# Performance work log

Hardware: AMD Instinct MI355X
Metric: run time of the kernel (lower is better)

The kernel has to match this reference:

```python
import jax, jax.numpy as jnp
import numpy as np

N_HEAD = 16

def setup_inputs() -> dict:
    key = jax.random.key(0)
    ks = jax.random.split(key, 5)
    B, S, D = 2, 2048, 1024
    x = jax.random.normal(ks[0], (B, S, D), dtype=jnp.float32)
    w_attn = jax.random.normal(ks[1], (3 * D, D), dtype=jnp.float32) * 0.02
    b_attn = jax.random.normal(ks[2], (3 * D,), dtype=jnp.float32) * 0.02
    w_proj = jax.random.normal(ks[3], (D, D), dtype=jnp.float32) * 0.02
    b_proj = jax.random.normal(ks[4], (D,), dtype=jnp.float32) * 0.02
    return {"x": x, "w_attn": w_attn, "b_attn": b_attn, "w_proj": w_proj, "b_proj": b_proj}

def reference(x, w_attn, b_attn, w_proj, b_proj):
    B, S, D = x.shape
    H = N_HEAD
    hd = D // H
    # QKV projection (nn.Linear: x @ W^T + b)
    qkv = x @ w_attn.T + b_attn  # [B, S, 3D]
    q, k, v = jnp.split(qkv, 3, axis=2)
    q = q.reshape(B, S, H, hd).transpose(0, 2, 1, 3)  # [B, H, S, hd]
    k = k.reshape(B, S, H, hd).transpose(0, 2, 1, 3)
    v = v.reshape(B, S, H, hd).transpose(0, 2, 1, 3)
    scale = 1.0 / jnp.sqrt(jnp.asarray(hd, dtype=x.dtype))
    attn = jnp.einsum("bhqd,bhkd->bhqk", q, k) * scale  # [B, H, S, S]
    causal = jnp.tril(jnp.ones((S, S), dtype=bool))
    attn = jnp.where(causal[None, None], attn, -jnp.inf)
    attn = jax.nn.softmax(attn, axis=-1)
    y = jnp.einsum("bhqk,bhkd->bhqd", attn, v)  # [B, H, S, hd]
    y = y.transpose(0, 2, 1, 3).reshape(B, S, D)
    return y @ w_proj.T + b_proj
```

## Files before the change

### kernel.cpp

```cpp
#include <hip/hip_runtime.h>
#include <hip/hip_bf16.h>

#define S_LEN 2048
#define DMODEL 1024
#define NHEAD 16
#define HD 64

typedef short short8 __attribute__((ext_vector_type(8)));
typedef short short4_t __attribute__((ext_vector_type(4)));
typedef float f32x4 __attribute__((ext_vector_type(4)));

__device__ inline unsigned short f2bf(float f) {
    union { float f; unsigned int u; } c;
    c.f = f;
    unsigned int r = c.u + 0x7fffu + ((c.u >> 16) & 1u);
    return (unsigned short)(r >> 16);
}

__global__ __launch_bounds__(256) void cast_f32_bf16(
    const float* __restrict__ in, short* __restrict__ out, int n8)
{
    int i = blockIdx.x * 256 + threadIdx.x;
    if (i < n8) {
        float4 a = ((const float4*)in)[2 * i];
        float4 b = ((const float4*)in)[2 * i + 1];
        short8 o;
        o[0] = (short)f2bf(a.x); o[1] = (short)f2bf(a.y);
        o[2] = (short)f2bf(a.z); o[3] = (short)f2bf(a.w);
        o[4] = (short)f2bf(b.x); o[5] = (short)f2bf(b.y);
        o[6] = (short)f2bf(b.z); o[7] = (short)f2bf(b.w);
        ((short8*)out)[i] = o;
    }
}

template<bool QKV>
__global__ __launch_bounds__(256) void gemm_mfma(
    const short* __restrict__ A, const short* __restrict__ W,
    const float* __restrict__ bias, float* __restrict__ C,
    int N, int K,
    short* __restrict__ qo, short* __restrict__ ko, short* __restrict__ vo)
{
    __shared__ __align__(16) short Ash[128 * 64];
    __shared__ __align__(16) short Bsh[128 * 64];

    const int tid = threadIdx.x;
    const int l = tid & 63;
    const int wid = tid >> 6;
    const int wr = wid >> 1, wc = wid & 1;
    const int n0 = blockIdx.x << 7, m0 = blockIdx.y << 7;

    const short* Abase = A + (size_t)m0 * K;
    const short* Wbase = W + (size_t)n0 * K;

    f32x4 acc[4][4];
    #pragma unroll
    for (int i = 0; i < 4; ++i)
        #pragma unroll
        for (int j = 0; j < 4; ++j)
            acc[i][j] = (f32x4)0.0f;

    short8 sa[4], sb[4];
    int rrow[4], rcol[4];
    #pragma unroll
    for (int i = 0; i < 4; ++i) {
        int chunk = i * 256 + tid;
        rrow[i] = chunk >> 3;
        rcol[i] = (chunk & 7) << 3;
    }

    #pragma unroll
    for (int i = 0; i < 4; ++i) {
        sa[i] = *(const short8*)(Abase + (size_t)rrow[i] * K + rcol[i]);
        sb[i] = *(const short8*)(Wbase + (size_t)rrow[i] * K + rcol[i]);
    }

    const int NT = K >> 6;
    for (int kt = 0; kt < NT; ++kt) {
        __syncthreads();
        #pragma unroll
        for (int i = 0; i < 4; ++i) {
            *(short8*)&Ash[rrow[i] * 64 + rcol[i]] = sa[i];
            *(short8*)&Bsh[rrow[i] * 64 + rcol[i]] = sb[i];
        }
        __syncthreads();
        if (kt + 1 < NT) {
            const int k0 = (kt + 1) << 6;
            #pragma unroll
            for (int i = 0; i < 4; ++i) {
                sa[i] = *(const short8*)(Abase + (size_t)rrow[i] * K + k0 + rcol[i]);
                sb[i] = *(const short8*)(Wbase + (size_t)rrow[i] * K + k0 + rcol[i]);
            }
        }
        #pragma unroll
        for (int kk = 0; kk < 2; ++kk) {
            short8 af[4], bf[4];
            const int kof = kk * 32 + ((l >> 4) << 3);
            #pragma unroll
            for (int mi = 0; mi < 4; ++mi)
                af[mi] = *(const short8*)&Ash[(wr * 64 + mi * 16 + (l & 15)) * 64 + kof];
            #pragma unroll
            for (int ni = 0; ni < 4; ++ni)
                bf[ni] = *(const short8*)&Bsh[(wc * 64 + ni * 16 + (l & 15)) * 64 + kof];
            #pragma unroll
            for (int mi = 0; mi < 4; ++mi)
                #pragma unroll
                for (int ni = 0; ni < 4; ++ni)
                    acc[mi][ni] = __builtin_amdgcn_mfma_f32_16x16x32_bf16(
                        af[mi], bf[ni], acc[mi][ni], 0, 0, 0);
        }
    }

    #pragma unroll
    for (int ni = 0; ni < 4; ++ni) {
        const int col = n0 + wc * 64 + ni * 16 + (l & 15);
        const float bv = bias[col];
        if (QKV) {
            const int part = col >> 10;
            const int h = (col >> 6) & 15;
            const int e = col & 63;
            short* __restrict__ dst = part == 0 ? qo : (part == 1 ? ko : vo);
            #pragma unroll
            for (int mi = 0; mi < 4; ++mi) {
                #pragma unroll
                for (int r = 0; r < 4; ++r) {
                    int row = m0 + wr * 64 + mi * 16 + ((l >> 4) << 2) + r;
                    int b = row >> 11, s = row & (S_LEN - 1);
                    dst[((size_t)(b * NHEAD + h) * S_LEN + s) * HD + e] =
                        (short)f2bf(acc[mi][ni][r] + bv);
                }
            }
        } else {
            #pragma unroll
            for (int mi = 0; mi < 4; ++mi) {
                #pragma unroll
                for (int r = 0; r < 4; ++r) {
                    int row = m0 + wr * 64 + mi * 16 + ((l >> 4) << 2) + r;
                    C[(size_t)row * N + col] = acc[mi][ni][r] + bv;
                }
            }
        }
    }
}

__global__ __launch_bounds__(256) void transpose_v(
    const short* __restrict__ vin, short* __restrict__ vout)
{
    __shared__ short t[64][72];
    const int tid = threadIdx.x;
    const int bh = blockIdx.x >> 5;
    const int s0 = (blockIdx.x & 31) << 6;
    const size_t ibase = (size_t)bh * S_LEN * HD;
    const size_t obase = (size_t)bh * HD * S_LEN;
    const int r = tid >> 3, c8 = (tid & 7) << 3;

    #pragma unroll
    for (int p = 0; p < 2; ++p) {
        short8 v = *(const short8*)&vin[ibase + (size_t)(s0 + r + p * 32) * HD + c8];
        *(short8*)&t[r + p * 32][c8] = v;
    }
    __syncthreads();
    #pragma unroll
    for (int p = 0; p < 2; ++p) {
        const int e = r + p * 32;
        short8 o;
        #pragma unroll
        for (int i = 0; i < 8; ++i) o[i] = t[c8 + i][e];
        *(short8*)&vout[obase + (size_t)e * S_LEN + s0 + c8] = o;
    }
}

__global__ __launch_bounds__(256) void flash_attn_mfma(
    const short* __restrict__ q, const short* __restrict__ k,
    const short* __restrict__ vt, short* __restrict__ yb)
{
    __shared__ __align__(16) short Ks[64 * 64];
    __shared__ __align__(16) short Vs[64 * 64];

    const int tid = threadIdx.x;
    const int l = tid & 63;
    const int w = tid >> 6;
    const int h4 = l >> 4;
    const int c15 = l & 15;
    const int bid = blockIdx.x;
    const int qt = 31 - (bid >> 5);
    const int bh = bid & 31;
    const int q0 = qt << 6;
    const int myq = q0 + (w << 4) + c15;

    const size_t kbase = (size_t)bh * S_LEN * HD;
    const size_t vbase = (size_t)bh * HD * S_LEN;

    short8 qf[2];
    {
        const short* qrow = q + kbase + (size_t)myq * HD;
        qf[0] = *(const short8*)(qrow + (h4 << 3));
        qf[1] = *(const short8*)(qrow + 32 + (h4 << 3));
    }

    f32x4 accO[4];
    #pragma unroll
    for (int i = 0; i < 4; ++i) accO[i] = (f32x4)0.0f;
    float mr = -1e30f, lr = 0.0f;

    const int srow0 = tid >> 3, scol = tid & 7;
    short8 kreg[2], vreg[2];
    #pragma unroll
    for (int p = 0; p < 2; ++p) {
        kreg[p] = *(const short8*)(k + kbase + (size_t)(srow0 + p * 32) * HD + scol * 8);
        vreg[p] = *(const short8*)(vt + vbase + (size_t)(srow0 + p * 32) * S_LEN + scol * 8);
    }

    const int ntiles = qt + 1;
    for (int t = 0; t < ntiles; ++t) {
        __syncthreads();
        #pragma unroll
        for (int p = 0; p < 2; ++p) {
            const int row = srow0 + p * 32;
            const int sc = (scol ^ (row & 7)) << 3;
            *(short8*)&Ks[row * 64 + sc] = kreg[p];
            *(short8*)&Vs[row * 64 + sc] = vreg[p];
        }
        __syncthreads();
        if (t + 1 < ntiles) {
            const int kn = (t + 1) << 6;
            #pragma unroll
            for (int p = 0; p < 2; ++p) {
                kreg[p] = *(const short8*)(k + kbase + (size_t)(kn + srow0 + p * 32) * HD + scol * 8);
                vreg[p] = *(const short8*)(vt + vbase + (size_t)(srow0 + p * 32) * S_LEN + kn + scol * 8);
            }
        }

        f32x4 sacc[4];
        #pragma unroll
        for (int nt = 0; nt < 4; ++nt) sacc[nt] = (f32x4)0.0f;
        #pragma unroll
        for (int c = 0; c < 2; ++c) {
            const int kof = (c << 5) + (h4 << 3);
            #pragma unroll
            for (int nt = 0; nt < 4; ++nt) {
                const int keyrow = nt * 16 + c15;
                const short8 kf = *(const short8*)&Ks[keyrow * 64 + (kof ^ ((keyrow & 7) << 3))];
                sacc[nt] = __builtin_amdgcn_mfma_f32_16x16x32_bf16(kf, qf[c], sacc[nt], 0, 0, 0);
            }
        }

        float p16[16];
        const bool diag = (t == qt);
        #pragma unroll
        for (int nt = 0; nt < 4; ++nt)
            #pragma unroll
            for (int r = 0; r < 4; ++r) {
                float v = sacc[nt][r] * 0.125f;
                if (diag && (nt * 16 + (h4 << 2) + r > (w << 4) + c15))
                    v = -1e30f;
                p16[nt * 4 + r] = v;
            }

        float mx = p16[0];
        #pragma unroll
        for (int i = 1; i < 16; ++i) mx = fmaxf(mx, p16[i]);
        mx = fmaxf(mx, __shfl_xor(mx, 16, 64));
        mx = fmaxf(mx, __shfl_xor(mx, 32, 64));
        const float mnew = fmaxf(mr, mx);
        const float alpha = __expf(mr - mnew);
        mr = mnew;
        float rs = 0.0f;
        #pragma unroll
        for (int i = 0; i < 16; ++i) {
            p16[i] = __expf(p16[i] - mnew);
            rs += p16[i];
        }
        rs += __shfl_xor(rs, 16, 64);
        rs += __shfl_xor(rs, 32, 64);
        lr = lr * alpha + rs;
        #pragma unroll
        for (int et = 0; et < 4; ++et) accO[et] *= alpha;

        short8 pb[2];
        #pragma unroll
        for (int c = 0; c < 2; ++c)
            #pragma unroll
            for (int i = 0; i < 8; ++i)
                pb[c][i] = (short)f2bf(p16[8 * c + i]);

        #pragma unroll
        for (int c = 0; c < 2; ++c) {
            const int ch = (c << 2) + (h4 >> 1);
            const int halfo = (h4 & 1) << 2;
            #pragma unroll
            for (int et = 0; et < 4; ++et) {
                const int e = (et << 4) + c15;
                const int rb = e << 6;
                const int sw = e & 7;
                const short4_t va = *(const short4_t*)&Vs[rb + ((ch ^ sw) << 3) + halfo];
                const short4_t vb = *(const short4_t*)&Vs[rb + (((ch + 2) ^ sw) << 3) + halfo];
                const short8 vf = {va[0], va[1], va[2], va[3], vb[0], vb[1], vb[2], vb[3]};
                accO[et] = __builtin_amdgcn_mfma_f32_16x16x32_bf16(vf, pb[c], accO[et], 0, 0, 0);
            }
        }
    }

    const int bq = bh >> 4, hh = bh & 15;
    const float inv = 1.0f / lr;
    short* orow = yb + ((size_t)bq * S_LEN + myq) * DMODEL + hh * HD;
    #pragma unroll
    for (int et = 0; et < 4; ++et) {
        short4_t o;
        #pragma unroll
        for (int r = 0; r < 4; ++r) o[r] = (short)f2bf(accO[et][r] * inv);
        *(short4_t*)&orow[(et << 4) + (h4 << 2)] = o;
    }
}

extern "C" void kernel_launch(void* const* d_in, const int* in_sizes, int n_in,
                              void* d_out, int out_size, void* d_ws, size_t ws_size,
                              hipStream_t stream) {
    const float* x      = (const float*)d_in[0];
    const float* w_attn = (const float*)d_in[1];
    const float* b_attn = (const float*)d_in[2];
    const float* w_proj = (const float*)d_in[3];
    const float* b_proj = (const float*)d_in[4];
    float* out = (float*)d_out;

    const int B = 2;
    const int M = B * S_LEN;
    const size_t x_elems  = (size_t)M * DMODEL;
    const size_t wa_elems = (size_t)3 * DMODEL * DMODEL;
    const size_t wp_elems = (size_t)DMODEL * DMODEL;

    char* wsb = (char*)d_ws;
    short* qw  = (short*)(wsb);
    short* kw  = (short*)(wsb + (8u << 20));
    short* vw  = (short*)(wsb + (16u << 20));
    short* vtw = (short*)(wsb + (24u << 20));
    short* xb  = (short*)(wsb + (32u << 20));
    short* yb  = (short*)(wsb + (32u << 20));
    short* wab = (short*)(wsb + (40u << 20));
    short* wpb = (short*)(wsb + (40u << 20));

    cast_f32_bf16<<<dim3((int)(x_elems  / 8 / 256)), 256, 0, stream>>>(x, xb, (int)(x_elems / 8));
    cast_f32_bf16<<<dim3((int)(wa_elems / 8 / 256)), 256, 0, stream>>>(w_attn, wab, (int)(wa_elems / 8));

    dim3 g1(3 * DMODEL / 128, M / 128);
    gemm_mfma<true><<<g1, 256, 0, stream>>>(xb, wab, b_attn, nullptr,
                                            3 * DMODEL, DMODEL, qw, kw, vw);

    cast_f32_bf16<<<dim3((int)(wp_elems / 8 / 256)), 256, 0, stream>>>(w_proj, wpb, (int)(wp_elems / 8));
    transpose_v<<<dim3(2 * NHEAD * (S_LEN / 64)), 256, 0, stream>>>(vw, vtw);

    flash_attn_mfma<<<dim3(2 * NHEAD * (S_LEN / 64)), 256, 0, stream>>>(qw, kw, vtw, yb);

    dim3 g3(DMODEL / 128, M / 128);
    gemm_mfma<false><<<g3, 256, 0, stream>>>(yb, wpb, b_proj, out,
                                             DMODEL, DMODEL,
                                             nullptr, nullptr, nullptr);
}
```

Before: 200.7 us.

## Load GEMM and attention tiles directly into LDS and skip unneeded softmax rescales

Replaces register-staged global-to-LDS copies in both the GEMM and attention kernels with direct global_load_lds transfers, using an XOR swizzle applied on the global address side so the LDS layout stays conflict-free. This drops the register prefetch of the next tile, so loads are no longer overlapped with compute across iterations; each tile load is now waited on before compute. The GEMM LDS reads are updated to match the new swizzle. The online softmax skips the alpha rescale of the accumulator and running sum when no lane's max increased, using a wave-wide vote.

```diff
diff --git a/kernel.cpp b/kernel.cpp
--- a/kernel.cpp
+++ b/kernel.cpp
@@ -9,6 +9,11 @@
 typedef short short8 __attribute__((ext_vector_type(8)));
 typedef short short4_t __attribute__((ext_vector_type(4)));
 typedef float f32x4 __attribute__((ext_vector_type(4)));
+
+#define GLOAD_LDS16(gp, lp)                                        \
+    __builtin_amdgcn_global_load_lds(                              \
+        (__attribute__((address_space(1))) void*)(gp),             \
+        (__attribute__((address_space(3))) void*)(lp), 16, 0, 0)
 
 __device__ inline unsigned short f2bf(float f) {
     union { float f; unsigned int u; } c;
@@ -59,48 +64,40 @@
         for (int j = 0; j < 4; ++j)
             acc[i][j] = (f32x4)0.0f;
 
-    short8 sa[4], sb[4];
-    int rrow[4], rcol[4];
+    int rrow[4], scol[4];
     #pragma unroll
     for (int i = 0; i < 4; ++i) {
         int chunk = i * 256 + tid;
         rrow[i] = chunk >> 3;
-        rcol[i] = (chunk & 7) << 3;
-    }
-
-    #pragma unroll
-    for (int i = 0; i < 4; ++i) {
-        sa[i] = *(const short8*)(Abase + (size_t)rrow[i] * K + rcol[i]);
-        sb[i] = *(const short8*)(Wbase + (size_t)rrow[i] * K + rcol[i]);
+        scol[i] = ((chunk & 7) ^ (rrow[i] & 7)) << 3;
     }
 
     const int NT = K >> 6;
     for (int kt = 0; kt < NT; ++kt) {
+        const int k0 = kt << 6;
         __syncthreads();
         #pragma unroll
         for (int i = 0; i < 4; ++i) {
-            *(short8*)&Ash[rrow[i] * 64 + rcol[i]] = sa[i];
-            *(short8*)&Bsh[rrow[i] * 64 + rcol[i]] = sb[i];
+            GLOAD_LDS16(Abase + (size_t)rrow[i] * K + k0 + scol[i],
+                        &Ash[(i * 256 + wid * 64) * 8]);
+            GLOAD_LDS16(Wbase + (size_t)rrow[i] * K + k0 + scol[i],
+                        &Bsh[(i * 256 + wid * 64) * 8]);
         }
         __syncthreads();
-        if (kt + 1 < NT) {
-            const int k0 = (kt + 1) << 6;
-            #pragma unroll
-            for (int i = 0; i < 4; ++i) {
-                sa[i] = *(const short8*)(Abase + (size_t)rrow[i] * K + k0 + rcol[i]);
-                sb[i] = *(const short8*)(Wbase + (size_t)rrow[i] * K + k0 + rcol[i]);
-            }
-        }
         #pragma unroll
         for (int kk = 0; kk < 2; ++kk) {
             short8 af[4], bf[4];
-            const int kof = kk * 32 + ((l >> 4) << 3);
-            #pragma unroll
-            for (int mi = 0; mi < 4; ++mi)
-                af[mi] = *(const short8*)&Ash[(wr * 64 + mi * 16 + (l & 15)) * 64 + kof];
-            #pragma unroll
-            for (int ni = 0; ni < 4; ++ni)
-                bf[ni] = *(const short8*)&Bsh[(wc * 64 + ni * 16 + (l & 15)) * 64 + kof];
+            const int slotg = (kk << 2) + (l >> 4);
+            #pragma unroll
+            for (int mi = 0; mi < 4; ++mi) {
+                const int row = wr * 64 + mi * 16 + (l & 15);
+                af[mi] = *(const short8*)&Ash[row * 64 + ((slotg ^ (row & 7)) << 3)];
+            }
+            #pragma unroll
+            for (int ni = 0; ni < 4; ++ni) {
+                const int row = wc * 64 + ni * 16 + (l & 15);
+                bf[ni] = *(const short8*)&Bsh[row * 64 + ((slotg ^ (row & 7)) << 3)];
+            }
             #pragma unroll
             for (int mi = 0; mi < 4; ++mi)
                 #pragma unroll
@@ -202,33 +199,22 @@
     for (int i = 0; i < 4; ++i) accO[i] = (f32x4)0.0f;
     float mr = -1e30f, lr = 0.0f;
 
-    const int srow0 = tid >> 3, scol = tid & 7;
-    short8 kreg[2], vreg[2];
-    #pragma unroll
-    for (int p = 0; p < 2; ++p) {
-        kreg[p] = *(const short8*)(k + kbase + (size_t)(srow0 + p * 32) * HD + scol * 8);
-        vreg[p] = *(const short8*)(vt + vbase + (size_t)(srow0 + p * 32) * S_LEN + scol * 8);
-    }
+    const int sr = tid >> 3, slotL = tid & 7;
 
     const int ntiles = qt + 1;
     for (int t = 0; t < ntiles; ++t) {
+        const int kn = t << 6;
         __syncthreads();
         #pragma unroll
         for (int p = 0; p < 2; ++p) {
-            const int row = srow0 + p * 32;
-            const int sc = (scol ^ (row & 7)) << 3;
-            *(short8*)&Ks[row * 64 + sc] = kreg[p];
-            *(short8*)&Vs[row * 64 + sc] = vreg[p];
+            const int row = sr + p * 32;
+            const int ss = (slotL ^ (row & 7)) << 3;
+            GLOAD_LDS16(k + kbase + (size_t)(kn + row) * HD + ss,
+                        &Ks[(p * 256 + w * 64) * 8]);
+            GLOAD_LDS16(vt + vbase + (size_t)row * S_LEN + kn + ss,
+                        &Vs[(p * 256 + w * 64) * 8]);
         }
         __syncthreads();
-        if (t + 1 < ntiles) {
-            const int kn = (t + 1) << 6;
-            #pragma unroll
-            for (int p = 0; p < 2; ++p) {
-                kreg[p] = *(const short8*)(k + kbase + (size_t)(kn + srow0 + p * 32) * HD + scol * 8);
-                vreg[p] = *(const short8*)(vt + vbase + (size_t)(srow0 + p * 32) * S_LEN + kn + scol * 8);
-            }
-        }
 
         f32x4 sacc[4];
         #pragma unroll
@@ -261,20 +247,23 @@
         for (int i = 1; i < 16; ++i) mx = fmaxf(mx, p16[i]);
         mx = fmaxf(mx, __shfl_xor(mx, 16, 64));
         mx = fmaxf(mx, __shfl_xor(mx, 32, 64));
-        const float mnew = fmaxf(mr, mx);
-        const float alpha = __expf(mr - mnew);
-        mr = mnew;
+        if (!__all(mx <= mr)) {
+            const float mnew = fmaxf(mr, mx);
+            const float alpha = __expf(mr - mnew);
+            mr = mnew;
+            lr *= alpha;
+            #pragma unroll
+            for (int et = 0; et < 4; ++et) accO[et] *= alpha;
+        }
         float rs = 0.0f;
         #pragma unroll
         for (int i = 0; i < 16; ++i) {
-            p16[i] = __expf(p16[i] - mnew);
+            p16[i] = __expf(p16[i] - mr);
             rs += p16[i];
         }
         rs += __shfl_xor(rs, 16, 64);
         rs += __shfl_xor(rs, 32, 64);
-        lr = lr * alpha + rs;
-        #pragma unroll
-        for (int et = 0; et < 4; ++et) accO[et] *= alpha;
+        lr += rs;
 
         short8 pb[2];
         #pragma unroll
```

Measured after the change: 203.9 us. Within noise of the previous version (+1.6%).
